# Kernel optimization log

Hardware: AMD Instinct MI355X
Metric: run time of the kernel (lower is better)

## Reference

```python
import jax, jax.numpy as jnp
import numpy as np

B, T, N = 128, 1024, 256
IC_ENC_D, CI_ENC_D, IC_DIM = 256, 256, 128
CLIP = 5.0
CI_LAG = 1
VAR_MIN = 1e-4


def _gru_params(key, d_in, d):
    k1, k2, k3 = jax.random.split(key, 3)
    s = 1.0 / np.sqrt(d_in + d)
    Wk = jax.random.normal(k1, (d_in, 3 * d), jnp.float32) * s
    U = jax.random.normal(k2, (d, 3 * d), jnp.float32) * s
    # keras ones_zeros-style bias: ones on z gate, zeros elsewhere
    b = jnp.concatenate([jnp.ones((d,)), jnp.zeros((2 * d,))]).astype(jnp.float32)
    return Wk, U, b


def setup_inputs() -> dict:
    key = jax.random.key(0)
    ks = jax.random.split(key, 8)
    data = jax.random.normal(ks[0], (B, T, N), jnp.float32)
    ic_Wk_f, ic_U_f, ic_b_f = _gru_params(ks[1], N, IC_ENC_D)
    ic_Wk_b, ic_U_b, ic_b_b = _gru_params(ks[2], N, IC_ENC_D)
    ci_Wk_f, ci_U_f, ci_b_f = _gru_params(ks[3], N, CI_ENC_D)
    ci_Wk_b, ci_U_b, ci_b_b = _gru_params(ks[4], N, CI_ENC_D)
    ic_h0 = jnp.zeros((2, IC_ENC_D), jnp.float32)  # trainable h0 (fwd, bwd)
    ci_h0 = jnp.zeros((2, CI_ENC_D), jnp.float32)
    sd = 1.0 / np.sqrt(2 * IC_ENC_D)
    W_mean = jax.random.normal(ks[5], (2 * IC_ENC_D, IC_DIM), jnp.float32) * sd
    b_mean = jnp.zeros((IC_DIM,), jnp.float32)
    W_logvar = jax.random.normal(ks[6], (2 * IC_ENC_D, IC_DIM), jnp.float32) * sd
    b_logvar = jnp.zeros((IC_DIM,), jnp.float32)
    return dict(data=data,
                ic_Wk_f=ic_Wk_f, ic_U_f=ic_U_f, ic_b_f=ic_b_f,
                ic_Wk_b=ic_Wk_b, ic_U_b=ic_U_b, ic_b_b=ic_b_b, ic_h0=ic_h0,
                ci_Wk_f=ci_Wk_f, ci_U_f=ci_U_f, ci_b_f=ci_b_f,
                ci_Wk_b=ci_Wk_b, ci_U_b=ci_U_b, ci_b_b=ci_b_b, ci_h0=ci_h0,
                W_mean=W_mean, b_mean=b_mean, W_logvar=W_logvar, b_logvar=b_logvar)


def _gru_scan(x, h0, Wk, U, b):
    """Clipped GRU (keras gate order z,r,h; reset_after=False).
    x: [B,T,Din], h0: [B,D]. Returns (h_last [B,D], h_seq [B,T,D])."""
    D = h0.shape[-1]
    xproj = jnp.einsum('btd,dh->bth', x, Wk) + b  # [B,T,3D]
    xproj_t = jnp.swapaxes(xproj, 0, 1)           # [T,B,3D]

    def step(h, xt):
        zr = jax.nn.sigmoid(xt[:, :2 * D] + h @ U[:, :2 * D])
        z, r = zr[:, :D], zr[:, D:]
        hh = jnp.tanh(xt[:, 2 * D:] + (r * h) @ U[:, 2 * D:])
        hn = jnp.clip(z * h + (1.0 - z) * hh, -CLIP, CLIP)
        return hn, hn

    h_last, h_seq = jax.lax.scan(step, h0, xproj_t)
    return h_last, jnp.swapaxes(h_seq, 0, 1)


def _encoder(data, ic_Wk_f, ic_U_f, ic_b_f, ic_Wk_b, ic_U_b, ic_b_b, ic_h0,
             ci_Wk_f, ci_U_f, ci_b_f, ci_Wk_b, ci_U_b, ci_b_b, ci_h0,
             W_mean, b_mean, W_logvar, b_logvar):
    b = data.shape[0]
    # FP_LEN=0, IC_ENC_SEQ_LEN=0, CS_DIM=0 -> ic_enc_data = ci_enc_data = data
    h0f = jnp.tile(ic_h0[0:1], (b, 1))
    h0b = jnp.tile(ic_h0[1:2], (b, 1))
    hf, _ = _gru_scan(data, h0f, ic_Wk_f, ic_U_f, ic_b_f)
    hb, _ = _gru_scan(data[:, ::-1, :], h0b, ic_Wk_b, ic_U_b, ic_b_b)
    h_n = jnp.concatenate([hf, hb], axis=-1)  # Bidirectional merge 'concat'
    ic_mean = h_n @ W_mean + b_mean
    ic_logvar = h_n @ W_logvar + b_logvar
    ic_stddev = jnp.sqrt(jnp.exp(ic_logvar) + VAR_MIN)

    c0f = jnp.tile(ci_h0[0:1], (b, 1))
    c0b = jnp.tile(ci_h0[1:2], (b, 1))
    _, ci_fwd = _gru_scan(data, c0f, ci_Wk_f, ci_U_f, ci_b_f)
    _, ci_bwd_rev = _gru_scan(data[:, ::-1, :], c0b, ci_Wk_b, ci_U_b, ci_b_b)
    ci_bwd = ci_bwd_rev[:, ::-1, :]  # align backward outputs to time
    # ci_len = T (FP_LEN=0, IC_ENC_SEQ_LEN=0)
    ci_fwd_p = jnp.pad(ci_fwd, ((0, 0), (CI_LAG, 0), (0, 0)))[:, :T, :]
    ci_bwd_p = jnp.pad(ci_bwd, ((0, 0), (0, CI_LAG), (0, 0)))[:, -T:, :]
    ci = jnp.concatenate([ci_fwd_p, ci_bwd_p], axis=-1)  # [B,T,2*CI_ENC_D]
    return ic_mean, ic_stddev, ci


def reference(data, ic_Wk_f, ic_U_f, ic_b_f, ic_Wk_b, ic_U_b, ic_b_b, ic_h0,
              ci_Wk_f, ci_U_f, ci_b_f, ci_Wk_b, ci_U_b, ci_b_b, ci_h0,
              W_mean, b_mean, W_logvar, b_logvar):
    return _encoder(data, ic_Wk_f, ic_U_f, ic_b_f, ic_Wk_b, ic_U_b, ic_b_b, ic_h0,
                    ci_Wk_f, ci_U_f, ci_b_f, ci_Wk_b, ci_U_b, ci_b_b, ci_h0,
                    W_mean, b_mean, W_logvar, b_logvar)
```

## Files before the change

kernel.cpp:

```cpp
#include <hip/hip_runtime.h>
#include <hip/hip_bf16.h>
#include <cstdint>
#include <cstddef>

typedef _Float16 half8 __attribute__((ext_vector_type(8)));
typedef _Float16 half4 __attribute__((ext_vector_type(4)));
typedef float floatx4 __attribute__((ext_vector_type(4)));


#define WS_DATA16_OFF   0ull
#define WS_WKT_OFF      67108864ull
#define WS_UFRAG_OFF    68681728ull
#define WS_XPF_OFF      70254592ull
#define WS_HLAST_OFF    875560960ull

__device__ __forceinline__ void gload_lds16(const void* g, void* l) {
  __builtin_amdgcn_global_load_lds((const __attribute__((address_space(1))) void*)g,
                                   (__attribute__((address_space(3))) void*)l, 16, 0, 0);
}

__device__ __forceinline__ float sigmoidf_(float x) {
  return __builtin_amdgcn_rcpf(1.0f + __expf(-x));
}
__device__ __forceinline__ float tanhf_(float x) {
  return 1.0f - 2.0f * __builtin_amdgcn_rcpf(__expf(2.0f * x) + 1.0f);
}

__global__ __launch_bounds__(256) void k_cvt_data(const float* __restrict__ src, _Float16* __restrict__ dst) {
  int i = blockIdx.x * 256 + threadIdx.x;
  float4 v = ((const float4*)src)[i];
  half4 h;
  h[0] = (_Float16)v.x; h[1] = (_Float16)v.y; h[2] = (_Float16)v.z; h[3] = (_Float16)v.w;
  *(half4*)(dst + (size_t)i * 4) = h;
}

__global__ __launch_bounds__(256) void k_prep_wkt(const float* __restrict__ w0, const float* __restrict__ w1,
                                                  const float* __restrict__ w2, const float* __restrict__ w3,
                                                  _Float16* __restrict__ wkT) {
  int gid = blockIdx.x * 256 + threadIdx.x;
  int k8 = gid & 31;
  int n  = gid >> 5;
  int g  = n / 768;
  int j  = n - g * 768;
  const float* W = (g == 0) ? w0 : (g == 1) ? w1 : (g == 2) ? w2 : w3;
  _Float16* o = wkT + (size_t)n * 256 + k8 * 8;
#pragma unroll
  for (int i = 0; i < 8; ++i) o[i] = (_Float16)W[(size_t)(k8 * 8 + i) * 768 + j];
}

__global__ __launch_bounds__(256) void k_prep_ufrag(const float* __restrict__ u0, const float* __restrict__ u1,
                                                    const float* __restrict__ u2, const float* __restrict__ u3,
                                                    _Float16* __restrict__ uf) {
  int gid = blockIdx.x * 256 + threadIdx.x;
  int lane = gid & 63;
  int kt = (gid >> 6) & 7;
  int r  = gid >> 9;
  int ct = r % 48;
  int g  = r / 48;
  int q = lane >> 4, lc = lane & 15;
  const float* U = (g == 0) ? u0 : (g == 1) ? u1 : (g == 2) ? u2 : u3;
  half8 v;
#pragma unroll
  for (int jj = 0; jj < 8; ++jj) v[jj] = (_Float16)U[(size_t)(32 * kt + 8 * q + jj) * 768 + 16 * ct + lc];
  *(half8*)(uf + (size_t)gid * 8) = v;
}

__global__ __launch_bounds__(256) void k_gemm_xpf(const _Float16* __restrict__ wkT,
                                                  const _Float16* __restrict__ dat,
                                                  const float* __restrict__ b0, const float* __restrict__ b1,
                                                  const float* __restrict__ b2, const float* __restrict__ b3,
                                                  _Float16* __restrict__ xpf) {
  __shared__ _Float16 As[128 * 64];
  __shared__ _Float16 Bs[128 * 64];
  int tid = threadIdx.x;
  int jt = blockIdx.x;
  int t  = blockIdx.y;
  int m0 = jt * 128;
  int w = tid >> 6, lane = tid & 63, q = lane >> 4, lc = lane & 15;
  int wm = w >> 1, wn = w & 1;
  floatx4 acc[4][4] = {};
  const char* aBase = (const char*)wkT;
  const char* bBase = (const char*)dat;
  for (int kb = 0; kb < 4; ++kb) {
    int k0 = kb * 64;
#pragma unroll
    for (int i = 0; i < 4; ++i) {
      int fb = tid * 16 + i * 4096;
      int row = fb >> 7;
      int cb  = fb & 127;
      gload_lds16(aBase + (size_t)(m0 + row) * 512 + k0 * 2 + cb,
                  (char*)As + ((tid >> 6) << 10) + i * 4096);
      gload_lds16(bBase + ((size_t)row * 1024 + t) * 512 + k0 * 2 + cb,
                  (char*)Bs + ((tid >> 6) << 10) + i * 4096);
    }
    __syncthreads();
#pragma unroll
    for (int kk = 0; kk < 2; ++kk) {
      half8 af[4], bf[4];
#pragma unroll
      for (int mt = 0; mt < 4; ++mt) af[mt] = *(const half8*)&As[(wm * 64 + mt * 16 + lc) * 64 + kk * 32 + q * 8];
#pragma unroll
      for (int nt = 0; nt < 4; ++nt) bf[nt] = *(const half8*)&Bs[(wn * 64 + nt * 16 + lc) * 64 + kk * 32 + q * 8];
#pragma unroll
      for (int mt = 0; mt < 4; ++mt)
#pragma unroll
        for (int nt = 0; nt < 4; ++nt)
          acc[mt][nt] = __builtin_amdgcn_mfma_f32_16x16x32_f16(af[mt], bf[nt], acc[mt][nt], 0, 0, 0);
    }
    __syncthreads();
  }
  int g = m0 / 768;
  const float* bp = (g == 0) ? b0 : (g == 1) ? b1 : (g == 2) ? b2 : b3;
  int jl0 = (m0 - g * 768) + wm * 64;
#pragma unroll
  for (int mt = 0; mt < 4; ++mt) {
    int jl = jl0 + mt * 16 + 4 * q;
    floatx4 bias = *(const floatx4*)&bp[jl];
    int jq = jl >> 2;
#pragma unroll
    for (int nt = 0; nt < 4; ++nt) {
      int bg = 4 * wn + nt;
      size_t chunk = ((size_t)(g * 8 + bg) * 1024 + t) * 12288;
      half4 v;
#pragma unroll
      for (int r = 0; r < 4; ++r) v[r] = (_Float16)(acc[mt][nt][r] + bias[r]);
      *(half4*)&xpf[chunk + (size_t)(jq * 16 + lc) * 4] = v;
    }
  }
}

__global__ __launch_bounds__(512) __attribute__((amdgpu_waves_per_eu(2, 2)))
void k_recur(const _Float16* __restrict__ uf,
             const _Float16* __restrict__ xpf,
             const float* __restrict__ ich0, const float* __restrict__ cih0,
             float* __restrict__ out, float* __restrict__ hlast) {
  __shared__ _Float16 xt[2][2][12288];
  __shared__ _Float16 h_s[2][16][264];
  __shared__ _Float16 rh_s[16][264];
  __shared__ float    z_s[16][260];

  int tid = threadIdx.x;
  int w = tid >> 6, lane = tid & 63, q = lane >> 4, lc = lane & 15;
  int blk = blockIdx.x;
  int g = blk >> 3, bg = blk & 7;
  int b0g = bg * 16;

  half8 u1[4][8], u2[2][8];
#pragma unroll
  for (int nt = 0; nt < 4; ++nt)
#pragma unroll
    for (int kt = 0; kt < 8; ++kt)
      u1[nt][kt] = *(const half8*)(uf + (((size_t)(g * 48 + 4 * w + nt) * 8 + kt) * 64 + lane) * 8);
#pragma unroll
  for (int nt = 0; nt < 2; ++nt)
#pragma unroll
    for (int kt = 0; kt < 8; ++kt)
      u2[nt][kt] = *(const half8*)(uf + (((size_t)(g * 48 + 32 + 2 * w + nt) * 8 + kt) * 64 + lane) * 8);

  const float* h0 = (g == 0) ? ich0 : (g == 1) ? ich0 + 256 : (g == 2) ? cih0 : cih0 + 256;
  for (int i = tid; i < 16 * 256; i += 512) {
    int bb = i >> 8, dd = i & 255;
    h_s[0][bb][dd] = (_Float16)h0[dd];
  }
  {
    int bb = tid >> 5, c8 = (tid & 31) * 8;
    float4 z4 = {0.f, 0.f, 0.f, 0.f};
    if (g == 2) {
      float* p = out + 32768 + ((size_t)(b0g + bb) * 1024 + 0) * 512 + c8;
      *(float4*)p = z4; *(float4*)(p + 4) = z4;
    } else if (g == 3) {
      float* p = out + 32768 + ((size_t)(b0g + bb) * 1024 + 1023) * 512 + 256 + c8;
      *(float4*)p = z4; *(float4*)(p + 4) = z4;
    }
  }

  bool rev = (g & 1);
  const char* chunk = (const char*)(xpf + (size_t)(g * 8 + bg) * 1024 * 12288);

#pragma unroll
  for (int i = 0; i < 6; ++i) {
    int o = tid * 16 + i * 8192;
    int ls = (o >= 24576) ? 1 : 0;
    int row = rev ? (1023 - ls) : ls;
    gload_lds16(chunk + (size_t)row * 24576 + (o - ls * 24576),
                (char*)xt + ((tid >> 6) << 10) + i * 8192);
  }
  asm volatile("s_waitcnt vmcnt(0) lgkmcnt(0)" ::: "memory");
  __builtin_amdgcn_s_barrier();

  int cur = 0, xb = 0;
  for (int t = 0; t < 1024; ++t) {
    if (!(t & 1) && t < 1022) {
      int s = t + 2;
#pragma unroll
      for (int i = 0; i < 6; ++i) {
        int o = tid * 16 + i * 8192;
        int ls = (o >= 24576) ? 1 : 0;
        int row = rev ? (1023 - (s + ls)) : (s + ls);
        gload_lds16(chunk + (size_t)row * 24576 + (o - ls * 24576),
                    (char*)xt + (xb ^ 1) * 49152 + ((tid >> 6) << 10) + i * 8192);
      }
    }
    const _Float16* xcur = &xt[xb][t & 1][0];

    floatx4 acc[4];
#pragma unroll
    for (int nt = 0; nt < 4; ++nt) {
      int ct = 4 * w + nt;
      half4 xv = *(const half4*)&xcur[((ct * 4 + q) * 16 + lc) * 4];
#pragma unroll
      for (int r = 0; r < 4; ++r) acc[nt][r] = (float)xv[r];
    }
#pragma unroll
    for (int kt = 0; kt < 8; ++kt) {
      half8 hb = *(const half8*)&h_s[cur][lc][kt * 32 + q * 8];
#pragma unroll
      for (int nt = 0; nt < 4; ++nt)
        acc[nt] = __builtin_amdgcn_mfma_f32_16x16x32_f16(u1[nt][kt], hb, acc[nt], 0, 0, 0);
    }
    if (w < 4) {
#pragma unroll
      for (int nt = 0; nt < 4; ++nt) {
        int j = 64 * w + 16 * nt + 4 * q;
        floatx4 zv;
#pragma unroll
        for (int r = 0; r < 4; ++r) zv[r] = sigmoidf_(acc[nt][r]);
        *(floatx4*)&z_s[lc][j] = zv;
      }
    } else {
#pragma unroll
      for (int nt = 0; nt < 4; ++nt) {
        int j = 64 * (w - 4) + 16 * nt + 4 * q;
        half4 hv = *(const half4*)&h_s[cur][lc][j];
        half4 rv;
#pragma unroll
        for (int r = 0; r < 4; ++r) rv[r] = (_Float16)(sigmoidf_(acc[nt][r]) * (float)hv[r]);
        *(half4*)&rh_s[lc][j] = rv;
      }
    }
    asm volatile("s_waitcnt lgkmcnt(0)" ::: "memory");
    __builtin_amdgcn_s_barrier();

    floatx4 acc2[2];
#pragma unroll
    for (int nt = 0; nt < 2; ++nt) {
      int ct = 32 + 2 * w + nt;
      half4 xv = *(const half4*)&xcur[((ct * 4 + q) * 16 + lc) * 4];
#pragma unroll
      for (int r = 0; r < 4; ++r) acc2[nt][r] = (float)xv[r];
    }
#pragma unroll
    for (int kt = 0; kt < 8; ++kt) {
      half8 rb = *(const half8*)&rh_s[lc][kt * 32 + q * 8];
#pragma unroll
      for (int nt = 0; nt < 2; ++nt)
        acc2[nt] = __builtin_amdgcn_mfma_f32_16x16x32_f16(u2[nt][kt], rb, acc2[nt], 0, 0, 0);
    }
    half4 hn16[2];
    floatx4 hnf[2];
#pragma unroll
    for (int nt = 0; nt < 2; ++nt) {
      int j = 32 * w + 16 * nt + 4 * q;
      half4 hv = *(const half4*)&h_s[cur][lc][j];
      floatx4 zv = *(const floatx4*)&z_s[lc][j];
#pragma unroll
      for (int r = 0; r < 4; ++r) {
        float th = tanhf_(acc2[nt][r]);
        float v = zv[r] * (float)hv[r] + (1.0f - zv[r]) * th;
        v = fminf(fmaxf(v, -5.0f), 5.0f);
        hnf[nt][r] = v;
        hn16[nt][r] = (_Float16)v;
      }
    }
    if (g >= 2) {
      int trow; bool valid;
      if (g == 2) { trow = t + 1;   valid = (t < 1023); }
      else        { trow = 1022 - t; valid = (t <= 1022); }
      if (valid) {
        float* p = out + 32768 + ((size_t)(b0g + lc) * 1024 + trow) * 512
                 + ((g == 3) ? 256 : 0) + 32 * w + 4 * q;
        *(floatx4*)p = hnf[0];
        *(floatx4*)(p + 16) = hnf[1];
      }
    }
#pragma unroll
    for (int nt = 0; nt < 2; ++nt) {
      int j = 32 * w + 16 * nt + 4 * q;
      *(half4*)&h_s[cur ^ 1][lc][j] = hn16[nt];
    }
    asm volatile("s_waitcnt lgkmcnt(0)" ::: "memory");
    if (t & 1) {
      if (g >= 2) asm volatile("s_waitcnt vmcnt(4)" ::: "memory");
      else        asm volatile("s_waitcnt vmcnt(0)" ::: "memory");
    }
    __builtin_amdgcn_s_barrier();
    cur ^= 1;
    xb ^= (t & 1);
  }
  if (g < 2) {
    int bb = tid >> 5, c8 = (tid & 31) * 8;
    half8 hv = *(const half8*)&h_s[0][bb][c8];
    float* p = hlast + ((size_t)g * 128 + b0g + bb) * 256 + c8;
#pragma unroll
    for (int r = 0; r < 8; ++r) p[r] = (float)hv[r];
  }
}

__global__ __launch_bounds__(256) void k_head(const float* __restrict__ hlast,
                                              const float* __restrict__ Wm, const float* __restrict__ bm,
                                              const float* __restrict__ Wl, const float* __restrict__ bl,
                                              float* __restrict__ out) {
  __shared__ float hn[512];
  int b = blockIdx.x, tid = threadIdx.x;
  hn[tid]       = hlast[(size_t)b * 256 + tid];
  hn[256 + tid] = hlast[32768 + (size_t)b * 256 + tid];
  __syncthreads();
  if (tid < 128) {
    float a = bm[tid];
    for (int k = 0; k < 512; ++k) a += hn[k] * Wm[(size_t)k * 128 + tid];
    out[b * 128 + tid] = a;
  } else {
    int j = tid - 128;
    float a = bl[j];
    for (int k = 0; k < 512; ++k) a += hn[k] * Wl[(size_t)k * 128 + j];
    out[16384 + b * 128 + j] = sqrtf(__expf(a) + 1e-4f);
  }
}

extern "C" void kernel_launch(void* const* d_in, const int* in_sizes, int n_in,
                              void* d_out, int out_size, void* d_ws, size_t ws_size,
                              hipStream_t stream) {
  const float* data  = (const float*)d_in[0];
  const float* icWkf = (const float*)d_in[1];
  const float* icUf  = (const float*)d_in[2];
  const float* icbf  = (const float*)d_in[3];
  const float* icWkb = (const float*)d_in[4];
  const float* icUb  = (const float*)d_in[5];
  const float* icbb  = (const float*)d_in[6];
  const float* ich0  = (const float*)d_in[7];
  const float* ciWkf = (const float*)d_in[8];
  const float* ciUf  = (const float*)d_in[9];
  const float* cibf  = (const float*)d_in[10];
  const float* ciWkb = (const float*)d_in[11];
  const float* ciUb  = (const float*)d_in[12];
  const float* cibb  = (const float*)d_in[13];
  const float* cih0  = (const float*)d_in[14];
  const float* Wm    = (const float*)d_in[15];
  const float* bm    = (const float*)d_in[16];
  const float* Wl    = (const float*)d_in[17];
  const float* bl    = (const float*)d_in[18];
  float* out = (float*)d_out;
  char* ws = (char*)d_ws;

  _Float16* data16 = (_Float16*)(ws + WS_DATA16_OFF);
  _Float16* wkT    = (_Float16*)(ws + WS_WKT_OFF);
  _Float16* uf     = (_Float16*)(ws + WS_UFRAG_OFF);
  _Float16* xpf    = (_Float16*)(ws + WS_XPF_OFF);
  float*    hlastp = (float*)(ws + WS_HLAST_OFF);

  hipLaunchKernelGGL(k_cvt_data, dim3(32768), dim3(256), 0, stream, data, data16);
  hipLaunchKernelGGL(k_prep_wkt, dim3(384), dim3(256), 0, stream, icWkf, icWkb, ciWkf, ciWkb, wkT);
  hipLaunchKernelGGL(k_prep_ufrag, dim3(384), dim3(256), 0, stream, icUf, icUb, ciUf, ciUb, uf);
  hipLaunchKernelGGL(k_gemm_xpf, dim3(24, 1024), dim3(256), 0, stream,
                     wkT, data16, icbf, icbb, cibf, cibb, xpf);
  hipLaunchKernelGGL(k_recur, dim3(32), dim3(512), 0, stream, uf, xpf, ich0, cih0, out, hlastp);
  hipLaunchKernelGGL(k_head, dim3(128), dim3(256), 0, stream, hlastp, Wm, bm, Wl, bl, out);
}
```

Measured before the change: 3.472 ms.

## Double recurrent kernel block to 1024 threads, halving per-wave MFMA tiles

The GRU recurrence kernel now runs 16 waves per block instead of 8. Each wave handles 2 gate tiles and 1 candidate tile per step instead of 4 and 2, so per-wave register use for the U fragments is halved and the serial MFMA chain each step gets shorter. Prefetch loads and the vmcnt waits are rescaled to match, and empty asm constraints pin U in VGPRs. The cost is more waves taking part in each per-step barrier and lower per-wave MFMA ILP.

```diff
diff --git a/kernel.cpp b/kernel.cpp
--- a/kernel.cpp
+++ b/kernel.cpp
@@ -129,7 +129,7 @@
   }
 }
 
-__global__ __launch_bounds__(512) __attribute__((amdgpu_waves_per_eu(2, 2)))
+__global__ __launch_bounds__(1024)
 void k_recur(const _Float16* __restrict__ uf,
              const _Float16* __restrict__ xpf,
              const float* __restrict__ ich0, const float* __restrict__ cih0,
@@ -145,24 +145,30 @@
   int g = blk >> 3, bg = blk & 7;
   int b0g = bg * 16;
 
-  half8 u1[4][8], u2[2][8];
-#pragma unroll
-  for (int nt = 0; nt < 4; ++nt)
+  half8 u1[2][8], u2[8];
+#pragma unroll
+  for (int nt = 0; nt < 2; ++nt)
 #pragma unroll
     for (int kt = 0; kt < 8; ++kt)
-      u1[nt][kt] = *(const half8*)(uf + (((size_t)(g * 48 + 4 * w + nt) * 8 + kt) * 64 + lane) * 8);
+      u1[nt][kt] = *(const half8*)(uf + (((size_t)(g * 48 + 2 * w + nt) * 8 + kt) * 64 + lane) * 8);
+#pragma unroll
+  for (int kt = 0; kt < 8; ++kt)
+    u2[kt] = *(const half8*)(uf + (((size_t)(g * 48 + 32 + w) * 8 + kt) * 64 + lane) * 8);
 #pragma unroll
   for (int nt = 0; nt < 2; ++nt)
 #pragma unroll
     for (int kt = 0; kt < 8; ++kt)
-      u2[nt][kt] = *(const half8*)(uf + (((size_t)(g * 48 + 32 + 2 * w + nt) * 8 + kt) * 64 + lane) * 8);
+      asm volatile("" : "+v"(u1[nt][kt]));
+#pragma unroll
+  for (int kt = 0; kt < 8; ++kt)
+    asm volatile("" : "+v"(u2[kt]));
 
   const float* h0 = (g == 0) ? ich0 : (g == 1) ? ich0 + 256 : (g == 2) ? cih0 : cih0 + 256;
-  for (int i = tid; i < 16 * 256; i += 512) {
+  for (int i = tid; i < 16 * 256; i += 1024) {
     int bb = i >> 8, dd = i & 255;
     h_s[0][bb][dd] = (_Float16)h0[dd];
   }
-  {
+  if (tid < 512) {
     int bb = tid >> 5, c8 = (tid & 31) * 8;
     float4 z4 = {0.f, 0.f, 0.f, 0.f};
     if (g == 2) {
@@ -178,12 +184,12 @@
   const char* chunk = (const char*)(xpf + (size_t)(g * 8 + bg) * 1024 * 12288);
 
 #pragma unroll
-  for (int i = 0; i < 6; ++i) {
-    int o = tid * 16 + i * 8192;
+  for (int i = 0; i < 3; ++i) {
+    int o = tid * 16 + i * 16384;
     int ls = (o >= 24576) ? 1 : 0;
     int row = rev ? (1023 - ls) : ls;
     gload_lds16(chunk + (size_t)row * 24576 + (o - ls * 24576),
-                (char*)xt + ((tid >> 6) << 10) + i * 8192);
+                (char*)xt + (w << 10) + i * 16384);
   }
   asm volatile("s_waitcnt vmcnt(0) lgkmcnt(0)" ::: "memory");
   __builtin_amdgcn_s_barrier();
@@ -193,20 +199,20 @@
     if (!(t & 1) && t < 1022) {
       int s = t + 2;
 #pragma unroll
-      for (int i = 0; i < 6; ++i) {
-        int o = tid * 16 + i * 8192;
+      for (int i = 0; i < 3; ++i) {
+        int o = tid * 16 + i * 16384;
         int ls = (o >= 24576) ? 1 : 0;
         int row = rev ? (1023 - (s + ls)) : (s + ls);
         gload_lds16(chunk + (size_t)row * 24576 + (o - ls * 24576),
-                    (char*)xt + (xb ^ 1) * 49152 + ((tid >> 6) << 10) + i * 8192);
+                    (char*)xt + (xb ^ 1) * 49152 + (w << 10) + i * 16384);
       }
     }
     const _Float16* xcur = &xt[xb][t & 1][0];
 
-    floatx4 acc[4];
-#pragma unroll
-    for (int nt = 0; nt < 4; ++nt) {
-      int ct = 4 * w + nt;
+    floatx4 acc[2];
+#pragma unroll
+    for (int nt = 0; nt < 2; ++nt) {
+      int ct = 2 * w + nt;
       half4 xv = *(const half4*)&xcur[((ct * 4 + q) * 16 + lc) * 4];
 #pragma unroll
       for (int r = 0; r < 4; ++r) acc[nt][r] = (float)xv[r];
@@ -215,13 +221,13 @@
     for (int kt = 0; kt < 8; ++kt) {
       half8 hb = *(const half8*)&h_s[cur][lc][kt * 32 + q * 8];
 #pragma unroll
-      for (int nt = 0; nt < 4; ++nt)
+      for (int nt = 0; nt < 2; ++nt)
         acc[nt] = __builtin_amdgcn_mfma_f32_16x16x32_f16(u1[nt][kt], hb, acc[nt], 0, 0, 0);
     }
-    if (w < 4) {
-#pragma unroll
-      for (int nt = 0; nt < 4; ++nt) {
-        int j = 64 * w + 16 * nt + 4 * q;
+    if (w < 8) {
+#pragma unroll
+      for (int nt = 0; nt < 2; ++nt) {
+        int j = 32 * w + 16 * nt + 4 * q;
         floatx4 zv;
 #pragma unroll
         for (int r = 0; r < 4; ++r) zv[r] = sigmoidf_(acc[nt][r]);
@@ -229,8 +235,8 @@
       }
     } else {
 #pragma unroll
-      for (int nt = 0; nt < 4; ++nt) {
-        int j = 64 * (w - 4) + 16 * nt + 4 * q;
+      for (int nt = 0; nt < 2; ++nt) {
+        int j = 32 * (w - 8) + 16 * nt + 4 * q;
         half4 hv = *(const half4*)&h_s[cur][lc][j];
         half4 rv;
 #pragma unroll
@@ -241,35 +247,31 @@
     asm volatile("s_waitcnt lgkmcnt(0)" ::: "memory");
     __builtin_amdgcn_s_barrier();
 
-    floatx4 acc2[2];
-#pragma unroll
-    for (int nt = 0; nt < 2; ++nt) {
-      int ct = 32 + 2 * w + nt;
+    floatx4 acc2;
+    {
+      int ct = 32 + w;
       half4 xv = *(const half4*)&xcur[((ct * 4 + q) * 16 + lc) * 4];
 #pragma unroll
-      for (int r = 0; r < 4; ++r) acc2[nt][r] = (float)xv[r];
+      for (int r = 0; r < 4; ++r) acc2[r] = (float)xv[r];
     }
 #pragma unroll
     for (int kt = 0; kt < 8; ++kt) {
       half8 rb = *(const half8*)&rh_s[lc][kt * 32 + q * 8];
-#pragma unroll
-      for (int nt = 0; nt < 2; ++nt)
-        acc2[nt] = __builtin_amdgcn_mfma_f32_16x16x32_f16(u2[nt][kt], rb, acc2[nt], 0, 0, 0);
-    }
-    half4 hn16[2];
-    floatx4 hnf[2];
-#pragma unroll
-    for (int nt = 0; nt < 2; ++nt) {
-      int j = 32 * w + 16 * nt + 4 * q;
+      acc2 = __builtin_amdgcn_mfma_f32_16x16x32_f16(u2[kt], rb, acc2, 0, 0, 0);
+    }
+    half4 hn16;
+    floatx4 hnf;
+    {
+      int j = 16 * w + 4 * q;
       half4 hv = *(const half4*)&h_s[cur][lc][j];
       floatx4 zv = *(const floatx4*)&z_s[lc][j];
 #pragma unroll
       for (int r = 0; r < 4; ++r) {
-        float th = tanhf_(acc2[nt][r]);
+        float th = tanhf_(acc2[r]);
         float v = zv[r] * (float)hv[r] + (1.0f - zv[r]) * th;
         v = fminf(fmaxf(v, -5.0f), 5.0f);
-        hnf[nt][r] = v;
-        hn16[nt][r] = (_Float16)v;
+        hnf[r] = v;
+        hn16[r] = (_Float16)v;
       }
     }
     if (g >= 2) {
@@ -278,26 +280,21 @@
       else        { trow = 1022 - t; valid = (t <= 1022); }
       if (valid) {
         float* p = out + 32768 + ((size_t)(b0g + lc) * 1024 + trow) * 512
-                 + ((g == 3) ? 256 : 0) + 32 * w + 4 * q;
-        *(floatx4*)p = hnf[0];
-        *(floatx4*)(p + 16) = hnf[1];
-      }
-    }
-#pragma unroll
-    for (int nt = 0; nt < 2; ++nt) {
-      int j = 32 * w + 16 * nt + 4 * q;
-      *(half4*)&h_s[cur ^ 1][lc][j] = hn16[nt];
-    }
+                 + ((g == 3) ? 256 : 0) + 16 * w + 4 * q;
+        *(floatx4*)p = hnf;
+      }
+    }
+    *(half4*)&h_s[cur ^ 1][lc][16 * w + 4 * q] = hn16;
     asm volatile("s_waitcnt lgkmcnt(0)" ::: "memory");
     if (t & 1) {
-      if (g >= 2) asm volatile("s_waitcnt vmcnt(4)" ::: "memory");
+      if (g >= 2) asm volatile("s_waitcnt vmcnt(2)" ::: "memory");
       else        asm volatile("s_waitcnt vmcnt(0)" ::: "memory");
     }
     __builtin_amdgcn_s_barrier();
     cur ^= 1;
     xb ^= (t & 1);
   }
-  if (g < 2) {
+  if (g < 2 && tid < 512) {
     int bb = tid >> 5, c8 = (tid & 31) * 8;
     half8 hv = *(const half8*)&h_s[0][bb][c8];
     float* p = hlast + ((size_t)g * 128 + b0g + bb) * 256 + c8;
@@ -363,6 +360,6 @@
   hipLaunchKernelGGL(k_prep_ufrag, dim3(384), dim3(256), 0, stream, icUf, icUb, ciUf, ciUb, uf);
   hipLaunchKernelGGL(k_gemm_xpf, dim3(24, 1024), dim3(256), 0, stream,
                      wkT, data16, icbf, icbb, cibf, cibb, xpf);
-  hipLaunchKernelGGL(k_recur, dim3(32), dim3(512), 0, stream, uf, xpf, ich0, cih0, out, hlastp);
+  hipLaunchKernelGGL(k_recur, dim3(32), dim3(1024), 0, stream, uf, xpf, ich0, cih0, out, hlastp);
   hipLaunchKernelGGL(k_head, dim3(128), dim3(256), 0, stream, hlastp, Wm, bm, Wl, bl, out);
 }
```

Measured after the change: 4.198 ms. +20.9%, slower.
